# Performance work log

Measured on AMD Instinct MI355X. Metric: run time of the kernel, lower is better.

The kernel has to match this reference:

```python
import jax, jax.numpy as jnp
import numpy as np

B, L, D, C, NQ, K, NL = 64, 1024, 256, 256, 10000, 4, 3


def setup_inputs() -> dict:
    key = jax.random.key(0)
    ks = jax.random.split(key, 10)
    s = 0.02
    return {
        "question_seq": jax.random.randint(ks[0], (B, L), 0, NQ),
        "correctness_seq": jax.random.randint(ks[1], (B, L), 0, 2),
        "cqc_seq": jax.random.uniform(ks[2], (B, L, C), dtype=jnp.float32),
        "Eq": jax.random.normal(ks[3], (NQ, D), dtype=jnp.float32) * s,
        "Ec": jax.random.normal(ks[4], (2, D), dtype=jnp.float32) * s,
        "W1_w": jax.random.normal(ks[5], (D, 4 * D + C), dtype=jnp.float32) * s,
        "W1_b": jnp.zeros((D,), jnp.float32),
        "W2_w": jax.random.normal(ks[6], (D, 4 * D + C), dtype=jnp.float32) * s,
        "W2_b": jnp.zeros((D,), jnp.float32),
        "conv_w": jax.random.normal(ks[7], (NL, K, D, 2 * D), dtype=jnp.float32) * s,  # WIO layout per layer
        "conv_b": jnp.zeros((NL, 2 * D), jnp.float32),
    }


def reference(question_seq, correctness_seq, cqc_seq, Eq, Ec,
              W1_w, W1_b, W2_w, W2_b, conv_w, conv_b):
    qe = Eq[question_seq]                      # [B,L,D]
    ce = Ec[correctness_seq]                   # [B,L,D]
    LIS = jnp.concatenate([qe, ce], axis=-1)   # [B,L,2D]

    # custom causal attention with double masking + renorm
    scores = jnp.einsum('bid,bjd->bij', qe, qe)            # [B,L,L]
    strict_upper = jnp.triu(jnp.ones((L, L), bool), k=1)
    scores = jnp.where(strict_upper, -jnp.inf, scores)
    W = jax.nn.softmax(scores, axis=-1)
    upper_incl = jnp.triu(jnp.ones((L, L), bool), k=0)
    W = jnp.where(upper_incl, 0.0, W)          # zero diag too
    W = W / (W.sum(axis=-1, keepdims=True) + 1e-8)
    HRP = jnp.einsum('bij,bjd->bid', W, LIS)   # [B,L,2D]

    H = jnp.concatenate([LIS, HRP, cqc_seq], axis=-1)      # [B,L,4D+C]
    Q = (H @ W1_w.T + W1_b) * jax.nn.sigmoid(H @ W2_w.T + W2_b)  # [B,L,D]

    # GLU-gated causal conv stack (dropout = identity in eval)
    dn = ('NWC', 'WIO', 'NWC')
    x = Q
    for i in range(NL):
        xp = jnp.pad(x, ((0, 0), (K - 1, 0), (0, 0)))      # left causal pad
        co = jax.lax.conv_general_dilated(xp, conv_w[i], (1,), 'VALID',
                                          dimension_numbers=dn) + conv_b[i]
        a, b = jnp.split(co, 2, axis=-1)
        x = a * jax.nn.sigmoid(b) + x

    predict = jax.nn.sigmoid(jnp.sum(x[:, :-1] * qe[:, 1:], axis=2))  # [B,L-1]
    return predict
```

## Files before the change

### kernel.cpp

```cpp
#include <hip/hip_runtime.h>
#include <hip/hip_bf16.h>

#define B_ 64
#define L_ 1024
#define D_ 256
#define M_ (B_*L_)

typedef __attribute__((ext_vector_type(8))) short s16x8;
typedef __attribute__((ext_vector_type(4))) float f32x4;

__device__ __forceinline__ float sigmoidf_(float z) { return 1.0f/(1.0f + __expf(-z)); }

__device__ __forceinline__ unsigned short f2bf(float x) {
  unsigned int u = __builtin_bit_cast(unsigned int, x);
  u += 0x7fffu + ((u >> 16) & 1u);
  return (unsigned short)(u >> 16);
}
__device__ __forceinline__ float bf2f(unsigned short u) {
  unsigned int x = ((unsigned int)u) << 16;
  return __builtin_bit_cast(float, x);
}
__device__ __forceinline__ uint4 pack8(const float* f) {
  union { unsigned short u[8]; uint4 v; } r;
  #pragma unroll
  for (int i = 0; i < 8; ++i) r.u[i] = f2bf(f[i]);
  return r.v;
}

__global__ __launch_bounds__(256) void k_embedT(const int* __restrict__ qs,
    const float* __restrict__ Eq, unsigned short* __restrict__ qe_bf,
    unsigned short* __restrict__ qeT) {
  __shared__ unsigned short tile[64*264];
  int jc = blockIdx.x;
  int b  = blockIdx.y;
  int t = threadIdx.x;
  int jr = t >> 2, seg = (t & 3) * 64;
  size_t bL = (size_t)b * L_;
  int q = qs[bL + jc*64 + jr];
  {
    const float4* src = (const float4*)(Eq + (size_t)q*D_ + seg);
    float f[8];
    #pragma unroll
    for (int m = 0; m < 8; ++m) {
      float4 v0 = src[2*m], v1 = src[2*m+1];
      f[0]=v0.x; f[1]=v0.y; f[2]=v0.z; f[3]=v0.w;
      f[4]=v1.x; f[5]=v1.y; f[6]=v1.z; f[7]=v1.w;
      *(uint4*)&tile[jr*264 + seg + m*8] = pack8(f);
    }
  }
  __syncthreads();
  {
    unsigned short* dst = qe_bf + (bL + jc*64 + jr)*D_ + seg;
    #pragma unroll
    for (int m = 0; m < 8; ++m)
      *(uint4*)(dst + m*8) = *(const uint4*)&tile[jr*264 + seg + m*8];
  }
  {
    int d = t;
    union { unsigned short u[64]; uint4 v[8]; } row;
    #pragma unroll
    for (int j = 0; j < 64; ++j) row.u[j] = tile[j*264 + d];
    unsigned short* dst = qeT + ((size_t)b*D_ + d)*L_ + jc*64;
    #pragma unroll
    for (int m = 0; m < 8; ++m) *(uint4*)(dst + m*8) = row.v[m];
  }
}

#define KSTR 264
#define TSTR 40
#define PSTR 40

__global__ __launch_bounds__(256) void k_attn_mfma(
    const unsigned short* __restrict__ qe_bf, const unsigned short* __restrict__ qeT,
    const int* __restrict__ cs, unsigned short* __restrict__ attq,
    float* __restrict__ stv, float* __restrict__ s1v) {
  __shared__ unsigned short sK[32*KSTR];
  __shared__ unsigned short sKT[256*TSTR];
  __shared__ unsigned short sP[64*PSTR];
  __shared__ float scj[32];
  __shared__ float redz[64], reds1[64], redzd[64];
  const int ord16[16] = {15,14,13,12, 8,9,10,11, 7,6,5,4, 0,1,2,3};
  int pos = blockIdx.x >> 6, b = blockIdx.x & 63;
  int t64 = ord16[pos];
  int i0 = t64 * 64;
  int t = threadIdx.x;
  int lane = t & 63, wv = t >> 6;
  int l15 = lane & 15, lq = lane >> 4;
  int koff = lq * 8;
  size_t bL = (size_t)b * L_;
  if (t < 64) { redz[t] = 0.f; reds1[t] = 0.f; redzd[t] = 0.f; }
  int mo = (wv & 1) * 16;
  int no = (wv >> 1) * 32;
  s16x8 qf[2][8];
  #pragma unroll
  for (int nt = 0; nt < 2; ++nt) {
    const unsigned short* qrow = qe_bf + (bL + i0 + no + nt*16 + l15)*D_;
    #pragma unroll
    for (int ks = 0; ks < 8; ++ks)
      qf[nt][ks] = *(const s16x8*)(qrow + ks*32 + koff);
  }
  int mo2 = (wv & 1) * 32;
  int do_ = (wv >> 1) * 128;
  f32x4 oacc[2][8];
  f32x4 zz = {0.f, 0.f, 0.f, 0.f};
  #pragma unroll
  for (int i = 0; i < 2; ++i)
    #pragma unroll
    for (int j = 0; j < 8; ++j) oacc[i][j] = zz;
  float rzs[2] = {0.f, 0.f}, rs1[2] = {0.f, 0.f}, rzd[2] = {0.f, 0.f};
  int njt = 2*t64 + 2;
  for (int jt = 0; jt < njt; ++jt) {
    int j0 = jt * 32;
    __syncthreads();
    {
      int jr = t >> 3, seg = (t & 7) * 32;
      const uint4* src = (const uint4*)(qe_bf + (bL + j0 + jr)*D_ + seg);
      #pragma unroll
      for (int m = 0; m < 4; ++m) *(uint4*)&sK[jr*KSTR + seg + m*8] = src[m];
    }
    {
      const uint4* src = (const uint4*)(qeT + ((size_t)b*D_ + t)*L_ + j0);
      #pragma unroll
      for (int m = 0; m < 4; ++m) *(uint4*)&sKT[t*TSTR + m*8] = src[m];
    }
    if (t < 32) scj[t] = (float)cs[bL + j0 + t];
    __syncthreads();
    f32x4 sacc[2]; sacc[0] = zz; sacc[1] = zz;
    #pragma unroll
    for (int ks = 0; ks < 8; ++ks) {
      s16x8 af = *(const s16x8*)&sK[(mo + l15)*KSTR + ks*32 + koff];
      sacc[0] = __builtin_amdgcn_mfma_f32_16x16x32_bf16(af, qf[0][ks], sacc[0], 0, 0, 0);
      sacc[1] = __builtin_amdgcn_mfma_f32_16x16x32_bf16(af, qf[1][ks], sacc[1], 0, 0, 0);
    }
    #pragma unroll
    for (int nt = 0; nt < 2; ++nt) {
      int ig = i0 + no + nt*16 + l15;
      union { unsigned short u[4]; unsigned long long q; } pk;
      #pragma unroll
      for (int r = 0; r < 4; ++r) {
        int jloc = mo + lq*4 + r;
        int jg = j0 + jloc;
        float ex = __expf(sacc[nt][r]);
        float e = (jg < ig) ? ex : 0.f;
        rzs[nt] += e;
        rs1[nt] = fmaf(e, scj[jloc], rs1[nt]);
        if (jg == ig) rzd[nt] += ex;
        pk.u[r] = f2bf(e);
      }
      *(unsigned long long*)&sP[(no + nt*16 + l15)*PSTR + mo + lq*4] = pk.q;
    }
    __syncthreads();
    s16x8 paf[2];
    #pragma unroll
    for (int mt = 0; mt < 2; ++mt)
      paf[mt] = *(const s16x8*)&sP[(mo2 + mt*16 + l15)*PSTR + koff];
    #pragma unroll
    for (int nt = 0; nt < 8; ++nt) {
      s16x8 bfr = *(const s16x8*)&sKT[(do_ + nt*16 + l15)*TSTR + koff];
      oacc[0][nt] = __builtin_amdgcn_mfma_f32_16x16x32_bf16(paf[0], bfr, oacc[0][nt], 0, 0, 0);
      oacc[1][nt] = __builtin_amdgcn_mfma_f32_16x16x32_bf16(paf[1], bfr, oacc[1][nt], 0, 0, 0);
    }
  }
  #pragma unroll
  for (int nt = 0; nt < 2; ++nt) {
    float z = rzs[nt], s1 = rs1[nt], zd = rzd[nt];
    z  += __shfl_xor(z, 16);  z  += __shfl_xor(z, 32);
    s1 += __shfl_xor(s1, 16); s1 += __shfl_xor(s1, 32);
    zd += __shfl_xor(zd, 16); zd += __shfl_xor(zd, 32);
    if (lq == 0) {
      atomicAdd(&redz[no + nt*16 + l15], z);
      atomicAdd(&reds1[no + nt*16 + l15], s1);
      atomicAdd(&redzd[no + nt*16 + l15], zd);
    }
  }
  __syncthreads();
  if (t < 64) {
    float z = redz[t], zd = redzd[t], s1 = reds1[t];
    float inv = 1.0f / (z + 1e-8f*(z + zd));
    stv[bL + i0 + t] = z * inv;
    s1v[bL + i0 + t] = s1 * inv;
    redz[t] = inv;
  }
  __syncthreads();
  #pragma unroll
  for (int mt = 0; mt < 2; ++mt)
    #pragma unroll
    for (int r = 0; r < 4; ++r) {
      int iloc = mo2 + mt*16 + lq*4 + r;
      float inv = redz[iloc];
      size_t base = (bL + i0 + iloc)*D_ + do_;
      #pragma unroll
      for (int nt = 0; nt < 8; ++nt)
        attq[base + nt*16 + l15] = f2bf(oacc[mt][nt][r] * inv);
    }
}

__global__ void k_cvt(const float* __restrict__ src, unsigned short* __restrict__ dst) {
  int i = blockIdx.x*256 + threadIdx.x;
  float4 v = ((const float4*)src)[i];
  union { unsigned short u[4]; uint2 q; } o;
  o.u[0] = f2bf(v.x); o.u[1] = f2bf(v.y); o.u[2] = f2bf(v.z); o.u[3] = f2bf(v.w);
  ((uint2*)dst)[i] = o.q;
}

__global__ __launch_bounds__(256) void k_cvt_convw(const float* __restrict__ w,
                                                   unsigned short* __restrict__ wT) {
  __shared__ unsigned short lds[64*72];
  int l = blockIdx.z;
  int k0 = blockIdx.x * 64;
  int oc0 = blockIdx.y * 64;
  const float* src = w + (size_t)l*524288;
  unsigned short* dst = wT + (size_t)l*524288;
  int t = threadIdx.x;
  #pragma unroll
  for (int it = 0; it < 4; ++it) {
    int kr = it*16 + (t >> 4);
    int oc = (t & 15)*4;
    float4 v = *(const float4*)(src + (size_t)(k0+kr)*512 + oc0 + oc);
    lds[(oc+0)*72 + kr] = f2bf(v.x);
    lds[(oc+1)*72 + kr] = f2bf(v.y);
    lds[(oc+2)*72 + kr] = f2bf(v.z);
    lds[(oc+3)*72 + kr] = f2bf(v.w);
  }
  __syncthreads();
  #pragma unroll
  for (int it = 0; it < 2; ++it) {
    int ocr = it*32 + (t >> 3);
    int kx = (t & 7)*8;
    *(uint4*)(dst + (size_t)(oc0+ocr)*1024 + k0 + kx) = *(const uint4*)&lds[ocr*72 + kx];
  }
}

#define SSTR 40

__global__ __launch_bounds__(256, 2) void k_mlp_mfma(
    const unsigned short* __restrict__ qe_bf, const unsigned short* __restrict__ attq,
    const float* __restrict__ stv, const float* __restrict__ s1v,
    const int* __restrict__ cs, const float* __restrict__ cqc,
    const float* __restrict__ Ec,
    const unsigned short* __restrict__ W1bf, const float* __restrict__ W1b,
    const unsigned short* __restrict__ W2bf, const float* __restrict__ W2b,
    unsigned short* __restrict__ out) {
  __shared__ unsigned short sA[128*SSTR], sB1[128*SSTR], sB2[128*SSTR];
  int t = threadIdx.x;
  int m0 = blockIdx.x * 128;
  int n0 = blockIdx.y * 128;
  int lr = t >> 1, kh = (t & 1) * 16;
  int arow = m0 + lr;
  int lane = t & 63, wv = t >> 6;
  int moff = (wv & 1) * 64, noff = (wv >> 1) * 64;
  int l15 = lane & 15, koff = (lane >> 4) * 8;
  f32x4 acc1[4][4], acc2[4][4];
  f32x4 zz = {0.f, 0.f, 0.f, 0.f};
  #pragma unroll
  for (int i = 0; i < 4; ++i)
    #pragma unroll
    for (int j = 0; j < 4; ++j) { acc1[i][j] = zz; acc2[i][j] = zz; }
  for (int k0 = 0; k0 < 1280; k0 += 32) {
    __syncthreads();
    {
      int seg = k0 >> 8;
      int ks = (k0 & 255) + kh;
      if (seg == 0 || seg == 2) {
        const uint4* p = (const uint4*)((seg == 0 ? qe_bf : attq) + (size_t)arow*D_ + ks);
        *(uint4*)&sA[lr*SSTR + kh]     = p[0];
        *(uint4*)&sA[lr*SSTR + kh + 8] = p[1];
      } else {
        float f[16];
        if (seg == 1) {
          int c = cs[arow];
          const float4* p = (const float4*)(Ec + (size_t)c*D_ + ks);
          #pragma unroll
          for (int m = 0; m < 4; ++m) { float4 v = p[m];
            f[4*m]=v.x; f[4*m+1]=v.y; f[4*m+2]=v.z; f[4*m+3]=v.w; }
        } else if (seg == 3) {
          float s1r = s1v[arow], s0r = stv[arow] - s1r;
          const float4* p1 = (const float4*)(Ec + D_ + ks);
          const float4* p0 = (const float4*)(Ec + ks);
          #pragma unroll
          for (int m = 0; m < 4; ++m) {
            float4 v1 = p1[m], v0 = p0[m];
            f[4*m]   = s1r*v1.x + s0r*v0.x;
            f[4*m+1] = s1r*v1.y + s0r*v0.y;
            f[4*m+2] = s1r*v1.z + s0r*v0.z;
            f[4*m+3] = s1r*v1.w + s0r*v0.w;
          }
        } else {
          const float4* p = (const float4*)(cqc + (size_t)arow*D_ + ks);
          #pragma unroll
          for (int m = 0; m < 4; ++m) { float4 v = p[m];
            f[4*m]=v.x; f[4*m+1]=v.y; f[4*m+2]=v.z; f[4*m+3]=v.w; }
        }
        *(uint4*)&sA[lr*SSTR + kh]     = pack8(f);
        *(uint4*)&sA[lr*SSTR + kh + 8] = pack8(f + 8);
      }
    }
    {
      const uint4* p1 = (const uint4*)(W1bf + (size_t)(n0+lr)*1280 + k0 + kh);
      const uint4* p2 = (const uint4*)(W2bf + (size_t)(n0+lr)*1280 + k0 + kh);
      *(uint4*)&sB1[lr*SSTR + kh]     = p1[0];
      *(uint4*)&sB1[lr*SSTR + kh + 8] = p1[1];
      *(uint4*)&sB2[lr*SSTR + kh]     = p2[0];
      *(uint4*)&sB2[lr*SSTR + kh + 8] = p2[1];
    }
    __syncthreads();
    s16x8 am[4], b1f[4], b2f[4];
    #pragma unroll
    for (int i = 0; i < 4; ++i)
      am[i] = *(const s16x8*)&sA[(moff + i*16 + l15)*SSTR + koff];
    #pragma unroll
    for (int j = 0; j < 4; ++j) {
      b1f[j] = *(const s16x8*)&sB1[(noff + j*16 + l15)*SSTR + koff];
      b2f[j] = *(const s16x8*)&sB2[(noff + j*16 + l15)*SSTR + koff];
    }
    #pragma unroll
    for (int i = 0; i < 4; ++i)
      #pragma unroll
      for (int j = 0; j < 4; ++j) {
        acc1[i][j] = __builtin_amdgcn_mfma_f32_16x16x32_bf16(am[i], b1f[j], acc1[i][j], 0, 0, 0);
        acc2[i][j] = __builtin_amdgcn_mfma_f32_16x16x32_bf16(am[i], b2f[j], acc2[i][j], 0, 0, 0);
      }
  }
  #pragma unroll
  for (int j = 0; j < 4; ++j) {
    int col = n0 + noff + j*16 + l15;
    float b1 = W1b[col], b2 = W2b[col];
    #pragma unroll
    for (int i = 0; i < 4; ++i) {
      int rbase = m0 + moff + i*16 + (lane >> 4)*4;
      #pragma unroll
      for (int r = 0; r < 4; ++r) {
        float z1 = acc1[i][j][r] + b1;
        float z2 = acc2[i][j][r] + b2;
        out[(size_t)(rbase + r)*D_ + col] = f2bf(z1 * sigmoidf_(z2));
      }
    }
  }
}

__global__ __launch_bounds__(256, 2) void k_conv_mfma(
    const unsigned short* __restrict__ xin, const unsigned short* __restrict__ wT,
    const float* __restrict__ bias, unsigned short* __restrict__ xout) {
  __shared__ unsigned short sA[128*SSTR], sBa[128*SSTR], sBb[128*SSTR];
  int t = threadIdx.x;
  int m0 = blockIdx.x * 128;
  int n0 = blockIdx.y * 128;
  int lr = t >> 1, kh = (t & 1) * 16;
  int arow = m0 + lr;
  int al = arow & (L_ - 1);
  int lane = t & 63, wv = t >> 6;
  int moff = (wv & 1) * 64, noff = (wv >> 1) * 64;
  int l15 = lane & 15, koff = (lane >> 4) * 8;
  f32x4 acca[4][4], accb[4][4];
  f32x4 zz = {0.f, 0.f, 0.f, 0.f};
  #pragma unroll
  for (int i = 0; i < 4; ++i)
    #pragma unroll
    for (int j = 0; j < 4; ++j) { acca[i][j] = zz; accb[i][j] = zz; }
  for (int k0 = 0; k0 < 1024; k0 += 32) {
    int tap = k0 >> 8;
    int ic = (k0 & 255) + kh;
    __syncthreads();
    {
      uint4 v0 = {0,0,0,0}, v1 = {0,0,0,0};
      if (al + tap >= 3) {
        const uint4* p = (const uint4*)(xin + (size_t)(arow + tap - 3)*D_ + ic);
        v0 = p[0]; v1 = p[1];
      }
      *(uint4*)&sA[lr*SSTR + kh]     = v0;
      *(uint4*)&sA[lr*SSTR + kh + 8] = v1;
    }
    {
      const uint4* pa = (const uint4*)(wT + (size_t)(n0+lr)*1024 + k0 + kh);
      const uint4* pb = (const uint4*)(wT + (size_t)(256+n0+lr)*1024 + k0 + kh);
      *(uint4*)&sBa[lr*SSTR + kh]     = pa[0];
      *(uint4*)&sBa[lr*SSTR + kh + 8] = pa[1];
      *(uint4*)&sBb[lr*SSTR + kh]     = pb[0];
      *(uint4*)&sBb[lr*SSTR + kh + 8] = pb[1];
    }
    __syncthreads();
    s16x8 am[4], baf[4], bbf[4];
    #pragma unroll
    for (int i = 0; i < 4; ++i)
      am[i] = *(const s16x8*)&sA[(moff + i*16 + l15)*SSTR + koff];
    #pragma unroll
    for (int j = 0; j < 4; ++j) {
      baf[j] = *(const s16x8*)&sBa[(noff + j*16 + l15)*SSTR + koff];
      bbf[j] = *(const s16x8*)&sBb[(noff + j*16 + l15)*SSTR + koff];
    }
    #pragma unroll
    for (int i = 0; i < 4; ++i)
      #pragma unroll
      for (int j = 0; j < 4; ++j) {
        acca[i][j] = __builtin_amdgcn_mfma_f32_16x16x32_bf16(am[i], baf[j], acca[i][j], 0, 0, 0);
        accb[i][j] = __builtin_amdgcn_mfma_f32_16x16x32_bf16(am[i], bbf[j], accb[i][j], 0, 0, 0);
      }
  }
  #pragma unroll
  for (int j = 0; j < 4; ++j) {
    int col = n0 + noff + j*16 + l15;
    float ba = bias[col], bb = bias[col + 256];
    #pragma unroll
    for (int i = 0; i < 4; ++i) {
      int rbase = m0 + moff + i*16 + (lane >> 4)*4;
      #pragma unroll
      for (int r = 0; r < 4; ++r) {
        size_t off = (size_t)(rbase + r)*D_ + col;
        float za = acca[i][j][r] + ba;
        float zb = accb[i][j][r] + bb;
        float res = bf2f(xin[off]);
        xout[off] = f2bf(za * sigmoidf_(zb) + res);
      }
    }
  }
}

__global__ void k_pred(const unsigned short* __restrict__ x, const int* __restrict__ qs,
                       const float* __restrict__ Eq, float* __restrict__ out) {
  int lane = threadIdx.x & 63;
  int wv = threadIdx.x >> 6;
  int oi = blockIdx.x*4 + wv;
  int b = oi / 1023;
  int tp = oi - b*1023;
  int row = b*L_ + tp;
  int q = qs[row + 1];
  ushort4 u = ((const ushort4*)(x + (size_t)row*D_))[lane];
  float4 qv = ((const float4*)(Eq + (size_t)q*D_))[lane];
  float s = bf2f(u.x)*qv.x + bf2f(u.y)*qv.y + bf2f(u.z)*qv.z + bf2f(u.w)*qv.w;
  #pragma unroll
  for (int off = 32; off; off >>= 1) s += __shfl_xor(s, off);
  if (lane == 0) out[oi] = sigmoidf_(s);
}

extern "C" void kernel_launch(void* const* d_in, const int* in_sizes, int n_in,
                              void* d_out, int out_size, void* d_ws, size_t ws_size,
                              hipStream_t stream) {
  const int*   qs  = (const int*)d_in[0];
  const int*   cs  = (const int*)d_in[1];
  const float* cqc = (const float*)d_in[2];
  const float* Eq  = (const float*)d_in[3];
  const float* Ec  = (const float*)d_in[4];
  const float* W1w = (const float*)d_in[5];
  const float* W1b = (const float*)d_in[6];
  const float* W2w = (const float*)d_in[7];
  const float* W2b = (const float*)d_in[8];
  const float* cw  = (const float*)d_in[9];
  const float* cb  = (const float*)d_in[10];
  float* out = (float*)d_out;

  char* w8 = (char*)d_ws;
  unsigned short* qe_bf = (unsigned short*)w8;
  unsigned short* qeT   = (unsigned short*)(w8 + ((size_t)32 << 20));
  unsigned short* attq  = (unsigned short*)(w8 + ((size_t)64 << 20));
  unsigned short* xA    = (unsigned short*)(w8 + ((size_t)96 << 20));
  float* stv = (float*)(w8 + ((size_t)128 << 20));
  float* s1v = stv + M_;
  unsigned short* W1bf = (unsigned short*)(s1v + M_);
  unsigned short* W2bf = W1bf + 256*1280;
  unsigned short* wT   = W2bf + 256*1280;
  unsigned short* xB = qeT;
  unsigned short* xC = qe_bf;
  unsigned short* xD = attq;

  k_cvt<<<(256*1280)/4/256, 256, 0, stream>>>(W1w, W1bf);
  k_cvt<<<(256*1280)/4/256, 256, 0, stream>>>(W2w, W2bf);
  k_cvt_convw<<<dim3(16, 8, 3), 256, 0, stream>>>(cw, wT);

  k_embedT<<<dim3(16, 64), 256, 0, stream>>>(qs, Eq, qe_bf, qeT);
  k_attn_mfma<<<1024, 256, 0, stream>>>(qe_bf, qeT, cs, attq, stv, s1v);
  k_mlp_mfma<<<dim3(M_/128, 2), 256, 0, stream>>>(qe_bf, attq, stv, s1v, cs, cqc, Ec,
                                                  W1bf, W1b, W2bf, W2b, xA);
  k_conv_mfma<<<dim3(M_/128, 2), 256, 0, stream>>>(xA, wT,           cb,        xB);
  k_conv_mfma<<<dim3(M_/128, 2), 256, 0, stream>>>(xB, wT + 524288,  cb + 512,  xC);
  k_conv_mfma<<<dim3(M_/128, 2), 256, 0, stream>>>(xC, wT + 1048576, cb + 1024, xD);
  k_pred<<<(B_*(L_-1))/4, 256, 0, stream>>>(xD, qs, Eq, out);
}
```

Before: 681.2 us.

## Load MFMA fragments directly from global memory, removing LDS staging in GEMMs

The MLP and causal-conv GEMM kernels no longer stage A and B tiles through shared memory with barriers. Each lane loads its MFMA operand fragments directly from global memory, including the on-the-fly fp32-to-bf16 conversion for the embedding and cqc segments. This removes the LDS round-trip and the two barriers per k-step. In exchange, waves in a block duplicate global loads, and reuse comes only from L1/L2 caching.

Result: slower. 1.090 ms (+60.0%).

```diff
diff --git a/kernel.cpp b/kernel.cpp
--- a/kernel.cpp
+++ b/kernel.cpp
@@ -22,6 +22,12 @@
 }
 __device__ __forceinline__ uint4 pack8(const float* f) {
   union { unsigned short u[8]; uint4 v; } r;
+  #pragma unroll
+  for (int i = 0; i < 8; ++i) r.u[i] = f2bf(f[i]);
+  return r.v;
+}
+__device__ __forceinline__ s16x8 pack8v(const float* f) {
+  union { unsigned short u[8]; s16x8 v; } r;
   #pragma unroll
   for (int i = 0; i < 8; ++i) r.u[i] = f2bf(f[i]);
   return r.v;
@@ -231,9 +237,7 @@
   }
 }
 
-#define SSTR 40
-
-__global__ __launch_bounds__(256, 2) void k_mlp_mfma(
+__global__ __launch_bounds__(256) void k_mlp_frag(
     const unsigned short* __restrict__ qe_bf, const unsigned short* __restrict__ attq,
     const float* __restrict__ stv, const float* __restrict__ s1v,
     const int* __restrict__ cs, const float* __restrict__ cqc,
@@ -241,15 +245,29 @@
     const unsigned short* __restrict__ W1bf, const float* __restrict__ W1b,
     const unsigned short* __restrict__ W2bf, const float* __restrict__ W2b,
     unsigned short* __restrict__ out) {
-  __shared__ unsigned short sA[128*SSTR], sB1[128*SSTR], sB2[128*SSTR];
   int t = threadIdx.x;
+  int lane = t & 63, wv = t >> 6;
   int m0 = blockIdx.x * 128;
   int n0 = blockIdx.y * 128;
-  int lr = t >> 1, kh = (t & 1) * 16;
-  int arow = m0 + lr;
-  int lane = t & 63, wv = t >> 6;
   int moff = (wv & 1) * 64, noff = (wv >> 1) * 64;
   int l15 = lane & 15, koff = (lane >> 4) * 8;
+  int mrow[4];
+  #pragma unroll
+  for (int i = 0; i < 4; ++i) mrow[i] = m0 + moff + i*16 + l15;
+  int ci[4]; float s1r[4], s0r[4];
+  #pragma unroll
+  for (int i = 0; i < 4; ++i) {
+    ci[i] = cs[mrow[i]];
+    float s1_ = s1v[mrow[i]];
+    s1r[i] = s1_; s0r[i] = stv[mrow[i]] - s1_;
+  }
+  const unsigned short* bp1[4]; const unsigned short* bp2[4];
+  #pragma unroll
+  for (int j = 0; j < 4; ++j) {
+    size_t nrow = (size_t)(n0 + noff + j*16 + l15);
+    bp1[j] = W1bf + nrow*1280 + koff;
+    bp2[j] = W2bf + nrow*1280 + koff;
+  }
   f32x4 acc1[4][4], acc2[4][4];
   f32x4 zz = {0.f, 0.f, 0.f, 0.f};
   #pragma unroll
@@ -257,61 +275,60 @@
     #pragma unroll
     for (int j = 0; j < 4; ++j) { acc1[i][j] = zz; acc2[i][j] = zz; }
   for (int k0 = 0; k0 < 1280; k0 += 32) {
-    __syncthreads();
-    {
-      int seg = k0 >> 8;
-      int ks = (k0 & 255) + kh;
-      if (seg == 0 || seg == 2) {
-        const uint4* p = (const uint4*)((seg == 0 ? qe_bf : attq) + (size_t)arow*D_ + ks);
-        *(uint4*)&sA[lr*SSTR + kh]     = p[0];
-        *(uint4*)&sA[lr*SSTR + kh + 8] = p[1];
-      } else {
-        float f[16];
-        if (seg == 1) {
-          int c = cs[arow];
-          const float4* p = (const float4*)(Ec + (size_t)c*D_ + ks);
-          #pragma unroll
-          for (int m = 0; m < 4; ++m) { float4 v = p[m];
-            f[4*m]=v.x; f[4*m+1]=v.y; f[4*m+2]=v.z; f[4*m+3]=v.w; }
-        } else if (seg == 3) {
-          float s1r = s1v[arow], s0r = stv[arow] - s1r;
-          const float4* p1 = (const float4*)(Ec + D_ + ks);
-          const float4* p0 = (const float4*)(Ec + ks);
-          #pragma unroll
-          for (int m = 0; m < 4; ++m) {
-            float4 v1 = p1[m], v0 = p0[m];
-            f[4*m]   = s1r*v1.x + s0r*v0.x;
-            f[4*m+1] = s1r*v1.y + s0r*v0.y;
-            f[4*m+2] = s1r*v1.z + s0r*v0.z;
-            f[4*m+3] = s1r*v1.w + s0r*v0.w;
-          }
-        } else {
-          const float4* p = (const float4*)(cqc + (size_t)arow*D_ + ks);
-          #pragma unroll
-          for (int m = 0; m < 4; ++m) { float4 v = p[m];
-            f[4*m]=v.x; f[4*m+1]=v.y; f[4*m+2]=v.z; f[4*m+3]=v.w; }
-        }
-        *(uint4*)&sA[lr*SSTR + kh]     = pack8(f);
-        *(uint4*)&sA[lr*SSTR + kh + 8] = pack8(f + 8);
-      }
-    }
-    {
-      const uint4* p1 = (const uint4*)(W1bf + (size_t)(n0+lr)*1280 + k0 + kh);
-      const uint4* p2 = (const uint4*)(W2bf + (size_t)(n0+lr)*1280 + k0 + kh);
-      *(uint4*)&sB1[lr*SSTR + kh]     = p1[0];
-      *(uint4*)&sB1[lr*SSTR + kh + 8] = p1[1];
-      *(uint4*)&sB2[lr*SSTR + kh]     = p2[0];
-      *(uint4*)&sB2[lr*SSTR + kh + 8] = p2[1];
-    }
-    __syncthreads();
-    s16x8 am[4], b1f[4], b2f[4];
-    #pragma unroll
-    for (int i = 0; i < 4; ++i)
-      am[i] = *(const s16x8*)&sA[(moff + i*16 + l15)*SSTR + koff];
+    int seg = k0 >> 8;
+    int ks = (k0 & 255) + koff;
+    s16x8 am[4];
+    if (seg == 0) {
+      #pragma unroll
+      for (int i = 0; i < 4; ++i)
+        am[i] = *(const s16x8*)(qe_bf + (size_t)mrow[i]*D_ + ks);
+    } else if (seg == 2) {
+      #pragma unroll
+      for (int i = 0; i < 4; ++i)
+        am[i] = *(const s16x8*)(attq + (size_t)mrow[i]*D_ + ks);
+    } else if (seg == 1) {
+      #pragma unroll
+      for (int i = 0; i < 4; ++i) {
+        const float4* p = (const float4*)(Ec + (size_t)ci[i]*D_ + ks);
+        float f[8];
+        float4 v0 = p[0], v1 = p[1];
+        f[0]=v0.x; f[1]=v0.y; f[2]=v0.z; f[3]=v0.w;
+        f[4]=v1.x; f[5]=v1.y; f[6]=v1.z; f[7]=v1.w;
+        am[i] = pack8v(f);
+      }
+    } else if (seg == 3) {
+      const float4* p1 = (const float4*)(Ec + D_ + ks);
+      const float4* p0 = (const float4*)(Ec + ks);
+      float4 e10 = p1[0], e11 = p1[1], e00 = p0[0], e01 = p0[1];
+      #pragma unroll
+      for (int i = 0; i < 4; ++i) {
+        float f[8];
+        f[0] = s1r[i]*e10.x + s0r[i]*e00.x;
+        f[1] = s1r[i]*e10.y + s0r[i]*e00.y;
+        f[2] = s1r[i]*e10.z + s0r[i]*e00.z;
+        f[3] = s1r[i]*e10.w + s0r[i]*e00.w;
+        f[4] = s1r[i]*e11.x + s0r[i]*e01.x;
+        f[5] = s1r[i]*e11.y + s0r[i]*e01.y;
+        f[6] = s1r[i]*e11.z + s0r[i]*e01.z;
+        f[7] = s1r[i]*e11.w + s0r[i]*e01.w;
+        am[i] = pack8v(f);
+      }
+    } else {
+      #pragma unroll
+      for (int i = 0; i < 4; ++i) {
+        const float4* p = (const float4*)(cqc + (size_t)mrow[i]*D_ + ks);
+        float f[8];
+        float4 v0 = p[0], v1 = p[1];
+        f[0]=v0.x; f[1]=v0.y; f[2]=v0.z; f[3]=v0.w;
+        f[4]=v1.x; f[5]=v1.y; f[6]=v1.z; f[7]=v1.w;
+        am[i] = pack8v(f);
+      }
+    }
+    s16x8 b1f[4], b2f[4];
     #pragma unroll
     for (int j = 0; j < 4; ++j) {
-      b1f[j] = *(const s16x8*)&sB1[(noff + j*16 + l15)*SSTR + koff];
-      b2f[j] = *(const s16x8*)&sB2[(noff + j*16 + l15)*SSTR + koff];
+      b1f[j] = *(const s16x8*)(bp1[j] + k0);
+      b2f[j] = *(const s16x8*)(bp2[j] + k0);
     }
     #pragma unroll
     for (int i = 0; i < 4; ++i)
@@ -338,55 +355,49 @@
   }
 }
 
-__global__ __launch_bounds__(256, 2) void k_conv_mfma(
+__global__ __launch_bounds__(256) void k_conv_frag(
     const unsigned short* __restrict__ xin, const unsigned short* __restrict__ wT,
     const float* __restrict__ bias, unsigned short* __restrict__ xout) {
-  __shared__ unsigned short sA[128*SSTR], sBa[128*SSTR], sBb[128*SSTR];
   int t = threadIdx.x;
+  int lane = t & 63, wv = t >> 6;
   int m0 = blockIdx.x * 128;
   int n0 = blockIdx.y * 128;
-  int lr = t >> 1, kh = (t & 1) * 16;
-  int arow = m0 + lr;
-  int al = arow & (L_ - 1);
-  int lane = t & 63, wv = t >> 6;
   int moff = (wv & 1) * 64, noff = (wv >> 1) * 64;
   int l15 = lane & 15, koff = (lane >> 4) * 8;
+  int mrow[4], al[4];
+  #pragma unroll
+  for (int i = 0; i < 4; ++i) {
+    mrow[i] = m0 + moff + i*16 + l15;
+    al[i] = mrow[i] & (L_ - 1);
+  }
+  const unsigned short* bpa[4]; const unsigned short* bpb[4];
+  #pragma unroll
+  for (int j = 0; j < 4; ++j) {
+    size_t nrow = (size_t)(n0 + noff + j*16 + l15);
+    bpa[j] = wT + nrow*1024 + koff;
+    bpb[j] = wT + (nrow + 256)*1024 + koff;
+  }
   f32x4 acca[4][4], accb[4][4];
   f32x4 zz = {0.f, 0.f, 0.f, 0.f};
+  s16x8 z8 = {0,0,0,0,0,0,0,0};
   #pragma unroll
   for (int i = 0; i < 4; ++i)
     #pragma unroll
     for (int j = 0; j < 4; ++j) { acca[i][j] = zz; accb[i][j] = zz; }
   for (int k0 = 0; k0 < 1024; k0 += 32) {
     int tap = k0 >> 8;
-    int ic = (k0 & 255) + kh;
-    __syncthreads();
-    {
-      uint4 v0 = {0,0,0,0}, v1 = {0,0,0,0};
-      if (al + tap >= 3) {
-        const uint4* p = (const uint4*)(xin + (size_t)(arow + tap - 3)*D_ + ic);
-        v0 = p[0]; v1 = p[1];
-      }
-      *(uint4*)&sA[lr*SSTR + kh]     = v0;
-      *(uint4*)&sA[lr*SSTR + kh + 8] = v1;
-    }
-    {
-      const uint4* pa = (const uint4*)(wT + (size_t)(n0+lr)*1024 + k0 + kh);
-      const uint4* pb = (const uint4*)(wT + (size_t)(256+n0+lr)*1024 + k0 + kh);
-      *(uint4*)&sBa[lr*SSTR + kh]     = pa[0];
-      *(uint4*)&sBa[lr*SSTR + kh + 8] = pa[1];
-      *(uint4*)&sBb[lr*SSTR + kh]     = pb[0];
-      *(uint4*)&sBb[lr*SSTR + kh + 8] = pb[1];
-    }
-    __syncthreads();
-    s16x8 am[4], baf[4], bbf[4];
+    int ic = (k0 & 255) + koff;
+    s16x8 am[4];
     #pragma unroll
     for (int i = 0; i < 4; ++i)
-      am[i] = *(const s16x8*)&sA[(moff + i*16 + l15)*SSTR + koff];
+      am[i] = (al[i] + tap >= 3)
+            ? *(const s16x8*)(xin + (size_t)(mrow[i] + tap - 3)*D_ + ic)
+            : z8;
+    s16x8 baf[4], bbf[4];
     #pragma unroll
     for (int j = 0; j < 4; ++j) {
-      baf[j] = *(const s16x8*)&sBa[(noff + j*16 + l15)*SSTR + koff];
-      bbf[j] = *(const s16x8*)&sBb[(noff + j*16 + l15)*SSTR + koff];
+      baf[j] = *(const s16x8*)(bpa[j] + k0);
+      bbf[j] = *(const s16x8*)(bpb[j] + k0);
     }
     #pragma unroll
     for (int i = 0; i < 4; ++i)
@@ -468,10 +479,10 @@
 
   k_embedT<<<dim3(16, 64), 256, 0, stream>>>(qs, Eq, qe_bf, qeT);
   k_attn_mfma<<<1024, 256, 0, stream>>>(qe_bf, qeT, cs, attq, stv, s1v);
-  k_mlp_mfma<<<dim3(M_/128, 2), 256, 0, stream>>>(qe_bf, attq, stv, s1v, cs, cqc, Ec,
+  k_mlp_frag<<<dim3(M_/128, 2), 256, 0, stream>>>(qe_bf, attq, stv, s1v, cs, cqc, Ec,
                                                   W1bf, W1b, W2bf, W2b, xA);
-  k_conv_mfma<<<dim3(M_/128, 2), 256, 0, stream>>>(xA, wT,           cb,        xB);
-  k_conv_mfma<<<dim3(M_/128, 2), 256, 0, stream>>>(xB, wT + 524288,  cb + 512,  xC);
-  k_conv_mfma<<<dim3(M_/128, 2), 256, 0, stream>>>(xC, wT + 1048576, cb + 1024, xD);
+  k_conv_frag<<<dim3(M_/128, 2), 256, 0, stream>>>(xA, wT,           cb,        xB);
+  k_conv_frag<<<dim3(M_/128, 2), 256, 0, stream>>>(xB, wT + 524288,  cb + 512,  xC);
+  k_conv_frag<<<dim3(M_/128, 2), 256, 0, stream>>>(xC, wT + 1048576, cb + 1024, xD);
   k_pred<<<(B_*(L_-1))/4, 256, 0, stream>>>(xD, qs, Eq, out);
 }
```

## Fold correctness-embedding GEMM segments into rank terms and stream pre-swizzled weights from registers

Applied to the files above, without the earlier changes.

The MLP drops the two K-segments that come from the 2-row correctness embedding (ce and the attention-weighted ce). Because Ec has only two rows, those products reduce to precomputed per-column dot products (tu) added in the epilogue, which cuts the MLP's K from 1280 to 768. Weights for both the MLP and the conv layers are pre-swizzled into MFMA fragment order so each wave loads its B fragments straight from global memory into registers, with no LDS staging. The A tile is double-buffered in LDS with one sync per K-step, and each wave now covers a 128x32 tile. The risks are higher register pressure from larger per-wave accumulators and repeated global reads of B fragments across blocks.

Result: faster. 570.4 us (-16.3%).

```diff
diff --git a/kernel.cpp b/kernel.cpp
--- a/kernel.cpp
+++ b/kernel.cpp
@@ -195,219 +195,262 @@
     }
 }
 
-__global__ void k_cvt(const float* __restrict__ src, unsigned short* __restrict__ dst) {
-  int i = blockIdx.x*256 + threadIdx.x;
-  float4 v = ((const float4*)src)[i];
-  union { unsigned short u[4]; uint2 q; } o;
-  o.u[0] = f2bf(v.x); o.u[1] = f2bf(v.y); o.u[2] = f2bf(v.z); o.u[3] = f2bf(v.w);
-  ((uint2*)dst)[i] = o.q;
-}
-
-__global__ __launch_bounds__(256) void k_cvt_convw(const float* __restrict__ w,
-                                                   unsigned short* __restrict__ wT) {
-  __shared__ unsigned short lds[64*72];
-  int l = blockIdx.z;
-  int k0 = blockIdx.x * 64;
-  int oc0 = blockIdx.y * 64;
-  const float* src = w + (size_t)l*524288;
-  unsigned short* dst = wT + (size_t)l*524288;
-  int t = threadIdx.x;
-  #pragma unroll
-  for (int it = 0; it < 4; ++it) {
-    int kr = it*16 + (t >> 4);
-    int oc = (t & 15)*4;
-    float4 v = *(const float4*)(src + (size_t)(k0+kr)*512 + oc0 + oc);
-    lds[(oc+0)*72 + kr] = f2bf(v.x);
-    lds[(oc+1)*72 + kr] = f2bf(v.y);
-    lds[(oc+2)*72 + kr] = f2bf(v.z);
-    lds[(oc+3)*72 + kr] = f2bf(v.w);
-  }
-  __syncthreads();
-  #pragma unroll
-  for (int it = 0; it < 2; ++it) {
-    int ocr = it*32 + (t >> 3);
-    int kx = (t & 7)*8;
-    *(uint4*)(dst + (size_t)(oc0+ocr)*1024 + k0 + kx) = *(const uint4*)&lds[ocr*72 + kx];
-  }
-}
-
-#define SSTR 40
-
-__global__ __launch_bounds__(256, 2) void k_mlp_mfma(
+__global__ void k_cvt_sw(const float* __restrict__ W, unsigned short* __restrict__ Wf) {
+  int tid = blockIdx.x*256 + threadIdx.x;
+  int lane = tid & 63;
+  int frag = tid >> 6;
+  int ks = frag % 24;
+  int nt = frag / 24;
+  int n = nt*16 + (lane & 15);
+  int seg = ks >> 3;
+  int kor = (seg == 0 ? 0 : (seg == 1 ? 512 : 1024)) + (ks & 7)*32 + (lane >> 4)*8;
+  const float4* src = (const float4*)(W + (size_t)n*1280 + kor);
+  float f[8];
+  float4 a = src[0], b = src[1];
+  f[0]=a.x; f[1]=a.y; f[2]=a.z; f[3]=a.w; f[4]=b.x; f[5]=b.y; f[6]=b.z; f[7]=b.w;
+  *(uint4*)(Wf + (size_t)frag*512 + (size_t)lane*8) = pack8(f);
+}
+
+__global__ void k_cvt_convw_sw(const float* __restrict__ w,
+                               unsigned short* __restrict__ wTf) {
+  int tid = blockIdx.x*256 + threadIdx.x;
+  int l = blockIdx.y;
+  int lane = tid & 63;
+  int frag = tid >> 6;
+  int ks = frag & 31, nt = frag >> 5;
+  int oc = nt*16 + (lane & 15);
+  int k = ks*32 + (lane >> 4)*8;
+  int tap = k >> 8, ic = k & 255;
+  const float* src = w + (size_t)l*524288 + ((size_t)(tap*256 + ic))*512 + oc;
+  float f[8];
+  #pragma unroll
+  for (int e = 0; e < 8; ++e) f[e] = src[(size_t)e*512];
+  *(uint4*)(wTf + (size_t)l*524288 + (size_t)frag*512 + (size_t)lane*8) = pack8(f);
+}
+
+__global__ __launch_bounds__(256) void k_tu(const float* __restrict__ Ec,
+    const float* __restrict__ W1w, const float* __restrict__ W2w,
+    float* __restrict__ tu) {
+  int n = blockIdx.x;
+  int wv = threadIdx.x >> 6, lane = threadIdx.x & 63;
+  int v = wv & 1;
+  int reg = (wv >> 1) ? 768 : 256;
+  const float* e  = Ec + (size_t)v*D_ + lane*4;
+  const float* w1 = W1w + (size_t)n*1280 + reg + lane*4;
+  const float* w2 = W2w + (size_t)n*1280 + reg + lane*4;
+  float d1 = 0.f, d2 = 0.f;
+  #pragma unroll
+  for (int m = 0; m < 4; ++m) {
+    float ev = e[m];
+    d1 = fmaf(ev, w1[m], d1);
+    d2 = fmaf(ev, w2[m], d2);
+  }
+  #pragma unroll
+  for (int off = 32; off; off >>= 1) { d1 += __shfl_xor(d1, off); d2 += __shfl_xor(d2, off); }
+  if (lane == 0) { tu[wv*256 + n] = d1; tu[1024 + wv*256 + n] = d2; }
+}
+
+__global__ __launch_bounds__(256, 2) void k_mlp_hyb(
     const unsigned short* __restrict__ qe_bf, const unsigned short* __restrict__ attq,
     const float* __restrict__ stv, const float* __restrict__ s1v,
     const int* __restrict__ cs, const float* __restrict__ cqc,
-    const float* __restrict__ Ec,
-    const unsigned short* __restrict__ W1bf, const float* __restrict__ W1b,
-    const unsigned short* __restrict__ W2bf, const float* __restrict__ W2b,
-    unsigned short* __restrict__ out) {
-  __shared__ unsigned short sA[128*SSTR], sB1[128*SSTR], sB2[128*SSTR];
+    const unsigned short* __restrict__ W1f, const float* __restrict__ W1b,
+    const unsigned short* __restrict__ W2f, const float* __restrict__ W2b,
+    const float* __restrict__ tu, unsigned short* __restrict__ out) {
+  __shared__ unsigned short sA[2][4096];
   int t = threadIdx.x;
+  int lane = t & 63, wv = t >> 6;
   int m0 = blockIdx.x * 128;
   int n0 = blockIdx.y * 128;
+  int l15 = lane & 15, lq = lane >> 4;
   int lr = t >> 1, kh = (t & 1) * 16;
   int arow = m0 + lr;
+  int sbase = ((lr >> 4)*64 + (kh >> 3)*16 + (lr & 15))*8;
+  int ntb = (n0 >> 4) + wv*2;
+  f32x4 acc1[8][2], acc2[8][2];
+  f32x4 zz = {0.f, 0.f, 0.f, 0.f};
+  #pragma unroll
+  for (int i = 0; i < 8; ++i) { acc1[i][0]=zz; acc1[i][1]=zz; acc2[i][0]=zz; acc2[i][1]=zz; }
+
+  auto stage_load = [&](int s, uint4* sr) {
+    int ks = (s & 7)*32 + kh;
+    if (s < 8) {
+      const uint4* p = (const uint4*)(qe_bf + (size_t)arow*D_ + ks);
+      sr[0] = p[0]; sr[1] = p[1];
+    } else if (s < 16) {
+      const uint4* p = (const uint4*)(attq + (size_t)arow*D_ + ks);
+      sr[0] = p[0]; sr[1] = p[1];
+    } else {
+      const uint4* p = (const uint4*)(cqc + (size_t)arow*D_ + ks);
+      sr[0] = p[0]; sr[1] = p[1]; sr[2] = p[2]; sr[3] = p[3];
+    }
+  };
+  auto stage_write = [&](int s, const uint4* sr, int b) {
+    unsigned short* dst = &sA[b][sbase];
+    if (s < 16) {
+      *(uint4*)dst = sr[0];
+      *(uint4*)(dst + 128) = sr[1];
+    } else {
+      const float* f = (const float*)sr;
+      *(uint4*)dst = pack8(f);
+      *(uint4*)(dst + 128) = pack8(f + 8);
+    }
+  };
+  auto loadB = [&](int s, s16x8* B1, s16x8* B2) {
+    #pragma unroll
+    for (int j = 0; j < 2; ++j) {
+      size_t off = ((size_t)(ntb + j)*24 + s)*512 + (size_t)lane*8;
+      B1[j] = *(const s16x8*)(W1f + off);
+      B2[j] = *(const s16x8*)(W2f + off);
+    }
+  };
+
+  uint4 sr[4];
+  s16x8 bc1[2], bc2[2];
+  stage_load(0, sr);
+  stage_write(0, sr, 0);
+  loadB(0, bc1, bc2);
+  __syncthreads();
+  for (int s = 0; s < 24; ++s) {
+    int nxt = s + 1;
+    uint4 srn[4];
+    s16x8 bn1[2], bn2[2];
+    if (nxt < 24) {
+      loadB(nxt, bn1, bn2);
+      stage_load(nxt, srn);
+    }
+    int cur = s & 1;
+    s16x8 am[8];
+    #pragma unroll
+    for (int mt = 0; mt < 8; ++mt)
+      am[mt] = *(const s16x8*)&sA[cur][(mt*64 + lane)*8];
+    #pragma unroll
+    for (int mt = 0; mt < 8; ++mt) {
+      acc1[mt][0] = __builtin_amdgcn_mfma_f32_16x16x32_bf16(am[mt], bc1[0], acc1[mt][0], 0, 0, 0);
+      acc1[mt][1] = __builtin_amdgcn_mfma_f32_16x16x32_bf16(am[mt], bc1[1], acc1[mt][1], 0, 0, 0);
+      acc2[mt][0] = __builtin_amdgcn_mfma_f32_16x16x32_bf16(am[mt], bc2[0], acc2[mt][0], 0, 0, 0);
+      acc2[mt][1] = __builtin_amdgcn_mfma_f32_16x16x32_bf16(am[mt], bc2[1], acc2[mt][1], 0, 0, 0);
+    }
+    if (nxt < 24) {
+      stage_write(nxt, srn, cur ^ 1);
+      bc1[0]=bn1[0]; bc1[1]=bn1[1]; bc2[0]=bn2[0]; bc2[1]=bn2[1];
+    }
+    __syncthreads();
+  }
+  int cols[2]; float cb1[2], cb2[2];
+  float t1a[2], t1b[2], u1a[2], u1b[2], t2a[2], t2b[2], u2a[2], u2b[2];
+  #pragma unroll
+  for (int j = 0; j < 2; ++j) {
+    int col = n0 + wv*32 + j*16 + l15;
+    cols[j] = col;
+    cb1[j] = W1b[col]; cb2[j] = W2b[col];
+    t1a[j] = tu[col];       t1b[j] = tu[256+col];
+    u1a[j] = tu[512+col];   u1b[j] = tu[768+col];
+    t2a[j] = tu[1024+col];  t2b[j] = tu[1280+col];
+    u2a[j] = tu[1536+col];  u2b[j] = tu[1792+col];
+  }
+  #pragma unroll
+  for (int mt = 0; mt < 8; ++mt) {
+    int rbase = m0 + mt*16 + lq*4;
+    #pragma unroll
+    for (int r = 0; r < 4; ++r) {
+      int row = rbase + r;
+      int c = cs[row];
+      float s1r = s1v[row];
+      float s0r = stv[row] - s1r;
+      #pragma unroll
+      for (int j = 0; j < 2; ++j) {
+        float z1 = acc1[mt][j][r] + cb1[j] + (c ? t1b[j] : t1a[j]) + s0r*u1a[j] + s1r*u1b[j];
+        float z2 = acc2[mt][j][r] + cb2[j] + (c ? t2b[j] : t2a[j]) + s0r*u2a[j] + s1r*u2b[j];
+        out[(size_t)row*D_ + cols[j]] = f2bf(z1 * sigmoidf_(z2));
+      }
+    }
+  }
+}
+
+__global__ __launch_bounds__(256, 2) void k_conv_hyb(
+    const unsigned short* __restrict__ xin, const unsigned short* __restrict__ wTf,
+    const float* __restrict__ bias, unsigned short* __restrict__ xout) {
+  __shared__ unsigned short sA[2][4096];
+  int t = threadIdx.x;
   int lane = t & 63, wv = t >> 6;
-  int moff = (wv & 1) * 64, noff = (wv >> 1) * 64;
-  int l15 = lane & 15, koff = (lane >> 4) * 8;
-  f32x4 acc1[4][4], acc2[4][4];
-  f32x4 zz = {0.f, 0.f, 0.f, 0.f};
-  #pragma unroll
-  for (int i = 0; i < 4; ++i)
-    #pragma unroll
-    for (int j = 0; j < 4; ++j) { acc1[i][j] = zz; acc2[i][j] = zz; }
-  for (int k0 = 0; k0 < 1280; k0 += 32) {
-    __syncthreads();
-    {
-      int seg = k0 >> 8;
-      int ks = (k0 & 255) + kh;
-      if (seg == 0 || seg == 2) {
-        const uint4* p = (const uint4*)((seg == 0 ? qe_bf : attq) + (size_t)arow*D_ + ks);
-        *(uint4*)&sA[lr*SSTR + kh]     = p[0];
-        *(uint4*)&sA[lr*SSTR + kh + 8] = p[1];
-      } else {
-        float f[16];
-        if (seg == 1) {
-          int c = cs[arow];
-          const float4* p = (const float4*)(Ec + (size_t)c*D_ + ks);
-          #pragma unroll
-          for (int m = 0; m < 4; ++m) { float4 v = p[m];
-            f[4*m]=v.x; f[4*m+1]=v.y; f[4*m+2]=v.z; f[4*m+3]=v.w; }
-        } else if (seg == 3) {
-          float s1r = s1v[arow], s0r = stv[arow] - s1r;
-          const float4* p1 = (const float4*)(Ec + D_ + ks);
-          const float4* p0 = (const float4*)(Ec + ks);
-          #pragma unroll
-          for (int m = 0; m < 4; ++m) {
-            float4 v1 = p1[m], v0 = p0[m];
-            f[4*m]   = s1r*v1.x + s0r*v0.x;
-            f[4*m+1] = s1r*v1.y + s0r*v0.y;
-            f[4*m+2] = s1r*v1.z + s0r*v0.z;
-            f[4*m+3] = s1r*v1.w + s0r*v0.w;
-          }
-        } else {
-          const float4* p = (const float4*)(cqc + (size_t)arow*D_ + ks);
-          #pragma unroll
-          for (int m = 0; m < 4; ++m) { float4 v = p[m];
-            f[4*m]=v.x; f[4*m+1]=v.y; f[4*m+2]=v.z; f[4*m+3]=v.w; }
-        }
-        *(uint4*)&sA[lr*SSTR + kh]     = pack8(f);
-        *(uint4*)&sA[lr*SSTR + kh + 8] = pack8(f + 8);
-      }
-    }
-    {
-      const uint4* p1 = (const uint4*)(W1bf + (size_t)(n0+lr)*1280 + k0 + kh);
-      const uint4* p2 = (const uint4*)(W2bf + (size_t)(n0+lr)*1280 + k0 + kh);
-      *(uint4*)&sB1[lr*SSTR + kh]     = p1[0];
-      *(uint4*)&sB1[lr*SSTR + kh + 8] = p1[1];
-      *(uint4*)&sB2[lr*SSTR + kh]     = p2[0];
-      *(uint4*)&sB2[lr*SSTR + kh + 8] = p2[1];
-    }
-    __syncthreads();
-    s16x8 am[4], b1f[4], b2f[4];
-    #pragma unroll
-    for (int i = 0; i < 4; ++i)
-      am[i] = *(const s16x8*)&sA[(moff + i*16 + l15)*SSTR + koff];
-    #pragma unroll
-    for (int j = 0; j < 4; ++j) {
-      b1f[j] = *(const s16x8*)&sB1[(noff + j*16 + l15)*SSTR + koff];
-      b2f[j] = *(const s16x8*)&sB2[(noff + j*16 + l15)*SSTR + koff];
-    }
-    #pragma unroll
-    for (int i = 0; i < 4; ++i)
-      #pragma unroll
-      for (int j = 0; j < 4; ++j) {
-        acc1[i][j] = __builtin_amdgcn_mfma_f32_16x16x32_bf16(am[i], b1f[j], acc1[i][j], 0, 0, 0);
-        acc2[i][j] = __builtin_amdgcn_mfma_f32_16x16x32_bf16(am[i], b2f[j], acc2[i][j], 0, 0, 0);
-      }
-  }
-  #pragma unroll
-  for (int j = 0; j < 4; ++j) {
-    int col = n0 + noff + j*16 + l15;
-    float b1 = W1b[col], b2 = W2b[col];
-    #pragma unroll
-    for (int i = 0; i < 4; ++i) {
-      int rbase = m0 + moff + i*16 + (lane >> 4)*4;
-      #pragma unroll
-      for (int r = 0; r < 4; ++r) {
-        float z1 = acc1[i][j][r] + b1;
-        float z2 = acc2[i][j][r] + b2;
-        out[(size_t)(rbase + r)*D_ + col] = f2bf(z1 * sigmoidf_(z2));
-      }
-    }
-  }
-}
-
-__global__ __launch_bounds__(256, 2) void k_conv_mfma(
-    const unsigned short* __restrict__ xin, const unsigned short* __restrict__ wT,
-    const float* __restrict__ bias, unsigned short* __restrict__ xout) {
-  __shared__ unsigned short sA[128*SSTR], sBa[128*SSTR], sBb[128*SSTR];
-  int t = threadIdx.x;
   int m0 = blockIdx.x * 128;
   int n0 = blockIdx.y * 128;
+  int l15 = lane & 15, lq = lane >> 4;
   int lr = t >> 1, kh = (t & 1) * 16;
   int arow = m0 + lr;
   int al = arow & (L_ - 1);
-  int lane = t & 63, wv = t >> 6;
-  int moff = (wv & 1) * 64, noff = (wv >> 1) * 64;
-  int l15 = lane & 15, koff = (lane >> 4) * 8;
-  f32x4 acca[4][4], accb[4][4];
+  int sbase = ((lr >> 4)*64 + (kh >> 3)*16 + (lr & 15))*8;
+  int nta = (n0 >> 4) + wv*2;
+  f32x4 acca[8][2], accb[8][2];
   f32x4 zz = {0.f, 0.f, 0.f, 0.f};
   #pragma unroll
-  for (int i = 0; i < 4; ++i)
-    #pragma unroll
-    for (int j = 0; j < 4; ++j) { acca[i][j] = zz; accb[i][j] = zz; }
-  for (int k0 = 0; k0 < 1024; k0 += 32) {
-    int tap = k0 >> 8;
-    int ic = (k0 & 255) + kh;
+  for (int i = 0; i < 8; ++i) { acca[i][0]=zz; acca[i][1]=zz; accb[i][0]=zz; accb[i][1]=zz; }
+
+  auto stage_load = [&](int s, uint4* sr) {
+    int tap = s >> 3;
+    uint4 z4 = {0,0,0,0};
+    sr[0] = z4; sr[1] = z4;
+    if (al + tap >= 3) {
+      const uint4* p = (const uint4*)(xin + (size_t)(arow + tap - 3)*D_ + (s & 7)*32 + kh);
+      sr[0] = p[0]; sr[1] = p[1];
+    }
+  };
+  auto loadB = [&](int s, s16x8* Ba, s16x8* Bb) {
+    #pragma unroll
+    for (int j = 0; j < 2; ++j) {
+      size_t off = ((size_t)(nta + j)*32 + s)*512 + (size_t)lane*8;
+      Ba[j] = *(const s16x8*)(wTf + off);
+      Bb[j] = *(const s16x8*)(wTf + off + 262144);
+    }
+  };
+
+  uint4 sr[2];
+  s16x8 bca[2], bcb[2];
+  stage_load(0, sr);
+  { unsigned short* dst = &sA[0][sbase]; *(uint4*)dst = sr[0]; *(uint4*)(dst+128) = sr[1]; }
+  loadB(0, bca, bcb);
+  __syncthreads();
+  for (int s = 0; s < 32; ++s) {
+    int nxt = s + 1;
+    uint4 srn[2];
+    s16x8 bna[2], bnb[2];
+    if (nxt < 32) {
+      loadB(nxt, bna, bnb);
+      stage_load(nxt, srn);
+    }
+    int cur = s & 1;
+    s16x8 am[8];
+    #pragma unroll
+    for (int mt = 0; mt < 8; ++mt)
+      am[mt] = *(const s16x8*)&sA[cur][(mt*64 + lane)*8];
+    #pragma unroll
+    for (int mt = 0; mt < 8; ++mt) {
+      acca[mt][0] = __builtin_amdgcn_mfma_f32_16x16x32_bf16(am[mt], bca[0], acca[mt][0], 0, 0, 0);
+      acca[mt][1] = __builtin_amdgcn_mfma_f32_16x16x32_bf16(am[mt], bca[1], acca[mt][1], 0, 0, 0);
+      accb[mt][0] = __builtin_amdgcn_mfma_f32_16x16x32_bf16(am[mt], bcb[0], accb[mt][0], 0, 0, 0);
+      accb[mt][1] = __builtin_amdgcn_mfma_f32_16x16x32_bf16(am[mt], bcb[1], accb[mt][1], 0, 0, 0);
+    }
+    if (nxt < 32) {
+      unsigned short* dst = &sA[cur ^ 1][sbase];
+      *(uint4*)dst = srn[0];
+      *(uint4*)(dst + 128) = srn[1];
+      bca[0]=bna[0]; bca[1]=bna[1]; bcb[0]=bnb[0]; bcb[1]=bnb[1];
+    }
     __syncthreads();
-    {
-      uint4 v0 = {0,0,0,0}, v1 = {0,0,0,0};
-      if (al + tap >= 3) {
-        const uint4* p = (const uint4*)(xin + (size_t)(arow + tap - 3)*D_ + ic);
-        v0 = p[0]; v1 = p[1];
-      }
-      *(uint4*)&sA[lr*SSTR + kh]     = v0;
-      *(uint4*)&sA[lr*SSTR + kh + 8] = v1;
-    }
-    {
-      const uint4* pa = (const uint4*)(wT + (size_t)(n0+lr)*1024 + k0 + kh);
-      const uint4* pb = (const uint4*)(wT + (size_t)(256+n0+lr)*1024 + k0 + kh);
-      *(uint4*)&sBa[lr*SSTR + kh]     = pa[0];
-      *(uint4*)&sBa[lr*SSTR + kh + 8] = pa[1];
-      *(uint4*)&sBb[lr*SSTR + kh]     = pb[0];
-      *(uint4*)&sBb[lr*SSTR + kh + 8] = pb[1];
-    }
-    __syncthreads();
-    s16x8 am[4], baf[4], bbf[4];
-    #pragma unroll
-    for (int i = 0; i < 4; ++i)
-      am[i] = *(const s16x8*)&sA[(moff + i*16 + l15)*SSTR + koff];
-    #pragma unroll
-    for (int j = 0; j < 4; ++j) {
-      baf[j] = *(const s16x8*)&sBa[(noff + j*16 + l15)*SSTR + koff];
-      bbf[j] = *(const s16x8*)&sBb[(noff + j*16 + l15)*SSTR + koff];
-    }
-    #pragma unroll
-    for (int i = 0; i < 4; ++i)
-      #pragma unroll
-      for (int j = 0; j < 4; ++j) {
-        acca[i][j] = __builtin_amdgcn_mfma_f32_16x16x32_bf16(am[i], baf[j], acca[i][j], 0, 0, 0);
-        accb[i][j] = __builtin_amdgcn_mfma_f32_16x16x32_bf16(am[i], bbf[j], accb[i][j], 0, 0, 0);
-      }
-  }
-  #pragma unroll
-  for (int j = 0; j < 4; ++j) {
-    int col = n0 + noff + j*16 + l15;
+  }
+  #pragma unroll
+  for (int j = 0; j < 2; ++j) {
+    int col = n0 + wv*32 + j*16 + l15;
     float ba = bias[col], bb = bias[col + 256];
     #pragma unroll
-    for (int i = 0; i < 4; ++i) {
-      int rbase = m0 + moff + i*16 + (lane >> 4)*4;
+    for (int mt = 0; mt < 8; ++mt) {
+      int rbase = m0 + mt*16 + lq*4;
       #pragma unroll
       for (int r = 0; r < 4; ++r) {
         size_t off = (size_t)(rbase + r)*D_ + col;
-        float za = acca[i][j][r] + ba;
-        float zb = accb[i][j][r] + bb;
+        float za = acca[mt][j][r] + ba;
+        float zb = accb[mt][j][r] + bb;
         float res = bf2f(xin[off]);
         xout[off] = f2bf(za * sigmoidf_(zb) + res);
       }
@@ -455,23 +498,25 @@
   unsigned short* xA    = (unsigned short*)(w8 + ((size_t)96 << 20));
   float* stv = (float*)(w8 + ((size_t)128 << 20));
   float* s1v = stv + M_;
-  unsigned short* W1bf = (unsigned short*)(s1v + M_);
-  unsigned short* W2bf = W1bf + 256*1280;
-  unsigned short* wT   = W2bf + 256*1280;
+  unsigned short* W1f = (unsigned short*)(s1v + M_);
+  unsigned short* W2f = W1f + 384*512;
+  unsigned short* wTf = W2f + 384*512;
+  float* tu = (float*)(wTf + (size_t)3*524288);
   unsigned short* xB = qeT;
   unsigned short* xC = qe_bf;
   unsigned short* xD = attq;
 
-  k_cvt<<<(256*1280)/4/256, 256, 0, stream>>>(W1w, W1bf);
-  k_cvt<<<(256*1280)/4/256, 256, 0, stream>>>(W2w, W2bf);
-  k_cvt_convw<<<dim3(16, 8, 3), 256, 0, stream>>>(cw, wT);
+  k_cvt_sw<<<96, 256, 0, stream>>>(W1w, W1f);
+  k_cvt_sw<<<96, 256, 0, stream>>>(W2w, W2f);
+  k_cvt_convw_sw<<<dim3(256, 3), 256, 0, stream>>>(cw, wTf);
+  k_tu<<<256, 256, 0, stream>>>(Ec, W1w, W2w, tu);
 
   k_embedT<<<dim3(16, 64), 256, 0, stream>>>(qs, Eq, qe_bf, qeT);
   k_attn_mfma<<<1024, 256, 0, stream>>>(qe_bf, qeT, cs, attq, stv, s1v);
-  k_mlp_mfma<<<dim3(M_/128, 2), 256, 0, stream>>>(qe_bf, attq, stv, s1v, cs, cqc, Ec,
-                                                  W1bf, W1b, W2bf, W2b, xA);
-  k_conv_mfma<<<dim3(M_/128, 2), 256, 0, stream>>>(xA, wT,           cb,        xB);
-  k_conv_mfma<<<dim3(M_/128, 2), 256, 0, stream>>>(xB, wT + 524288,  cb + 512,  xC);
-  k_conv_mfma<<<dim3(M_/128, 2), 256, 0, stream>>>(xC, wT + 1048576, cb + 1024, xD);
+  k_mlp_hyb<<<dim3(M_/128, 2), 256, 0, stream>>>(qe_bf, attq, stv, s1v, cs, cqc,
+                                                 W1f, W1b, W2f, W2b, tu, xA);
+  k_conv_hyb<<<dim3(M_/128, 2), 256, 0, stream>>>(xA, wTf,           cb,        xB);
+  k_conv_hyb<<<dim3(M_/128, 2), 256, 0, stream>>>(xB, wTf + 524288,  cb + 512,  xC);
+  k_conv_hyb<<<dim3(M_/128, 2), 256, 0, stream>>>(xC, wTf + 1048576, cb + 1024, xD);
   k_pred<<<(B_*(L_-1))/4, 256, 0, stream>>>(xD, qs, Eq, out);
 }
```
